# Performance work log

Measured on AMD Instinct MI355X. Metric: run time of the kernel, lower is better.

Reference implementation:

```python
import jax, jax.numpy as jnp
import numpy as np

GROUP_SIZE = 128
LORA_SCALING = 32.0 / 16.0  # lora_alpha / r


def _unpack_rows(q):
    # q: int32 [n, m] -> uint4 values [n*8, m], 8 nibbles per int32 along axis 0
    shifts = (jnp.arange(8, dtype=jnp.int32) * 4)
    vals = (q[:, None, :] >> shifts[None, :, None]) & 0xF
    return vals.reshape(q.shape[0] * 8, q.shape[1])


def _unpack_cols(q):
    # q: int32 [g, m] -> uint4 values [g, m*8], 8 nibbles per int32 along axis 1
    shifts = (jnp.arange(8, dtype=jnp.int32) * 4)
    vals = (q[:, :, None] >> shifts[None, None, :]) & 0xF
    return vals.reshape(q.shape[0], q.shape[1] * 8)


def setup_inputs() -> dict:
    key = jax.random.key(0)
    ks = jax.random.split(key, 6)
    in_f, out_f, tokens, r = 4096, 11008, 64, 16
    g = in_f // GROUP_SIZE  # 32 groups
    x = jax.random.normal(ks[0], (tokens, in_f), dtype=jnp.float32)
    qweight = jax.random.randint(ks[1], (in_f // 8, out_f), jnp.iinfo(jnp.int32).min, jnp.iinfo(jnp.int32).max, dtype=jnp.int32)
    qzeros = jax.random.randint(ks[2], (g, out_f // 8), jnp.iinfo(jnp.int32).min, jnp.iinfo(jnp.int32).max, dtype=jnp.int32)
    scales = jax.random.uniform(ks[3], (g, out_f), dtype=jnp.float32) * 0.01 + 0.001
    lora_A = jax.random.normal(ks[4], (r, in_f), dtype=jnp.float32) * 0.02
    lora_B = jax.random.normal(ks[5], (out_f, r), dtype=jnp.float32) * 0.02
    return {"x": x, "qweight": qweight, "qzeros": qzeros, "scales": scales,
            "lora_A": lora_A, "lora_B": lora_B}


def reference(x, qweight, qzeros, scales, lora_A, lora_B):
    in_f = qweight.shape[0] * 8
    # --- GPTQ int4 dequant ---
    wq = _unpack_rows(qweight).astype(jnp.float32)          # [in, out]
    zeros = (_unpack_cols(qzeros) + 1).astype(jnp.float32)  # [groups, out] (GPTQ +1 offset)
    g_idx = jnp.arange(in_f) // GROUP_SIZE                  # [in]
    W = scales[g_idx] * (wq - zeros[g_idx])                 # [in, out]
    # base quantized matmul
    result = x @ W                                          # [tokens, out]
    # --- LoRA adapter (single active adapter, dropout=0, tmp_weight=1) ---
    lora_out = (x @ lora_A.T) @ lora_B.T                    # [tokens, out]
    return result + lora_out * LORA_SCALING
```

## Files before the change

### kernel.cpp

```cpp
#include <hip/hip_runtime.h>
#include <stdint.h>

#define TOKENS 64
#define IN_F   4096
#define OUT_F  11008
#define RANK   16
#define GS     128
#define NG     32
#define ZCOLS  (OUT_F / 8)
#define LORA_SCALE 2.0f

using short8  = __attribute__((ext_vector_type(8))) short;
using float4v = __attribute__((ext_vector_type(4))) float;

static __device__ inline uint16_t f2bf(float f, float* back) {
    uint32_t u = __float_as_uint(f);
    uint32_t r = (u + 0x7FFFu + ((u >> 16) & 1u)) >> 16;
    *back = __uint_as_float(r << 16);
    return (uint16_t)r;
}

__global__ __launch_bounds__(256) void prep_kernel(
        const float* __restrict__ x,
        const float* __restrict__ loraA,
        uint4* __restrict__ xf4,
        float* __restrict__ xsumT,
        float* __restrict__ midT) {
    __shared__ float redg[256];
    __shared__ float redm[4][16];
    const int t    = blockIdx.x;
    const int tid  = threadIdx.x;
    const int lane = tid & 63;
    const int wv   = tid >> 6;

    float4 xv[4];
    const float4* xp = (const float4*)(x + (size_t)t * IN_F + tid * 16);
    #pragma unroll
    for (int i = 0; i < 4; ++i) xv[i] = xp[i];

    union { uint16_t u[16]; uint4 q[2]; } ob;
    float s = 0.f;
    #pragma unroll
    for (int i = 0; i < 4; ++i) {
        float b;
        ob.u[i * 4 + 0] = f2bf(xv[i].x, &b); s += b;
        ob.u[i * 4 + 1] = f2bf(xv[i].y, &b); s += b;
        ob.u[i * 4 + 2] = f2bf(xv[i].z, &b); s += b;
        ob.u[i * 4 + 3] = f2bf(xv[i].w, &b); s += b;
    }
    {
        const int mm = t >> 4, nn = t & 15;
        const int kchunk = tid >> 1;
        #pragma unroll
        for (int i = 0; i < 2; ++i) {
            const int qd = (tid * 2 + i) & 3;
            xf4[(size_t)((mm * 128 + kchunk) * 64 + qd * 16 + nn)] = ob.q[i];
        }
    }
    redg[tid] = s;

    float pj[16];
    #pragma unroll
    for (int j = 0; j < 16; ++j) {
        const float4* ap = (const float4*)(loraA + (size_t)j * IN_F + tid * 16);
        float ps = 0.f;
        #pragma unroll
        for (int i = 0; i < 4; ++i) {
            float4 a = ap[i];
            ps += a.x * xv[i].x + a.y * xv[i].y + a.z * xv[i].z + a.w * xv[i].w;
        }
        pj[j] = ps;
    }
    #pragma unroll
    for (int j = 0; j < 16; ++j) {
        #pragma unroll
        for (int off = 32; off; off >>= 1) pj[j] += __shfl_down(pj[j], off);
    }
    if (lane == 0) {
        #pragma unroll
        for (int j = 0; j < 16; ++j) redm[wv][j] = pj[j];
    }
    __syncthreads();
    if (tid < NG) {
        float g = 0.f;
        #pragma unroll
        for (int i = 0; i < 8; ++i) g += redg[tid * 8 + i];
        xsumT[tid * TOKENS + t] = g;
    }
    if (tid < 16)
        midT[tid * TOKENS + t] = redm[0][tid] + redm[1][tid] + redm[2][tid] + redm[3][tid];
}

__global__ __launch_bounds__(256) void lora_out_kernel(
        const float* __restrict__ midT,
        const float* __restrict__ loraB,
        float* __restrict__ out) {
    const int gid = blockIdx.x * 256 + threadIdx.x;
    const int t = gid / OUT_F;
    const int o = gid - t * OUT_F;
    const float4* b4 = (const float4*)(loraB + (size_t)o * RANK);
    float s = 0.f;
    #pragma unroll
    for (int i = 0; i < 4; ++i) {
        float4 b = b4[i];
        s += b.x * midT[(i * 4 + 0) * TOKENS + t];
        s += b.y * midT[(i * 4 + 1) * TOKENS + t];
        s += b.z * midT[(i * 4 + 2) * TOKENS + t];
        s += b.w * midT[(i * 4 + 3) * TOKENS + t];
    }
    out[gid] = s * LORA_SCALE;
}

#define LOADG(st, g) do {                                                       \
    _Pragma("unroll")                                                           \
    for (int mt = 0; mt < 2; ++mt)                                              \
        _Pragma("unroll")                                                       \
        for (int ks = 0; ks < 4; ++ks)                                          \
            A[st][mt * 4 + ks] =                                                \
                xf4[(size_t)(((mh * 2 + mt) * 128 + (g) * 4 + ks) * 64) + lane];\
    _Pragma("unroll")                                                           \
    for (int ks = 0; ks < 4; ++ks)                                              \
        _Pragma("unroll")                                                       \
        for (int nh = 0; nh < 2; ++nh)                                          \
            B[st][ks * 2 + nh] =                                                \
                qwc[(size_t)((g) * 16 + ks * 4 + quad) * OUT_F + nh * 16];      \
    _Pragma("unroll")                                                           \
    for (int mt = 0; mt < 2; ++mt)                                              \
        XS[st][mt] = *(const float4*)(xsumT + (g) * 64 +                        \
                                      (mh * 2 + mt) * 16 + quad * 4);           \
    _Pragma("unroll")                                                           \
    for (int nh = 0; nh < 2; ++nh) {                                            \
        S[st][nh] = scales[(size_t)(g) * OUT_F + col0 + nh * 16 + n];           \
        Z[st][nh] = qz[(size_t)(g) * ZCOLS + ((col0 + nh * 16 + n) >> 3)];      \
    }                                                                           \
} while (0)

#define COMPUTEG(st) do {                                                       \
    float4v accg[2][2];                                                         \
    _Pragma("unroll")                                                           \
    for (int mt = 0; mt < 2; ++mt)                                              \
        _Pragma("unroll")                                                       \
        for (int nh = 0; nh < 2; ++nh)                                          \
            accg[mt][nh] = (float4v){0.f, 0.f, 0.f, 0.f};                       \
    _Pragma("unroll")                                                           \
    for (int ks = 0; ks < 4; ++ks) {                                            \
        union { uint4 u; short8 s; } af0, af1;                                  \
        af0.u = A[st][ks];                                                      \
        af1.u = A[st][4 + ks];                                                  \
        _Pragma("unroll")                                                       \
        for (int nh = 0; nh < 2; ++nh) {                                        \
            uint32_t q  = B[st][ks * 2 + nh];                                   \
            uint32_t lo = q & 0x0F0F0F0Fu;                                      \
            uint32_t hi = (q >> 4) & 0x0F0F0F0Fu;                               \
            union { uint32_t u32[4]; short8 s8; } bf;                           \
            _Pragma("unroll")                                                   \
            for (int i = 0; i < 4; ++i)                                         \
                bf.u32[i] = __builtin_amdgcn_perm(hi, lo,                       \
                                0x0C040C00u + i * 0x00010001u) | 0x43004300u;   \
            accg[0][nh] = __builtin_amdgcn_mfma_f32_16x16x32_bf16(af0.s, bf.s8, \
                                                            accg[0][nh], 0, 0, 0);\
            accg[1][nh] = __builtin_amdgcn_mfma_f32_16x16x32_bf16(af1.s, bf.s8, \
                                                            accg[1][nh], 0, 0, 0);\
        }                                                                       \
    }                                                                           \
    _Pragma("unroll")                                                           \
    for (int nh = 0; nh < 2; ++nh) {                                            \
        const float zoff = (float)(((Z[st][nh] >>                               \
                        (((col0 + nh * 16 + n) & 7) * 4)) & 0xFu) + 129u);      \
        const float scl = S[st][nh];                                            \
        _Pragma("unroll")                                                       \
        for (int mt = 0; mt < 2; ++mt) {                                        \
            const float xr[4] = {XS[st][mt].x, XS[st][mt].y,                    \
                                 XS[st][mt].z, XS[st][mt].w};                   \
            _Pragma("unroll")                                                   \
            for (int r = 0; r < 4; ++r)                                         \
                acc[mt][nh][r] = fmaf(scl, fmaf(-zoff, xr[r],                   \
                                      accg[mt][nh][r]), acc[mt][nh][r]);        \
        }                                                                       \
    }                                                                           \
} while (0)

__global__ __launch_bounds__(256, 3) void main_kernel(
        const uint32_t* __restrict__ qw,
        const uint32_t* __restrict__ qz,
        const float* __restrict__ scales,
        const uint4* __restrict__ xf4,
        const float* __restrict__ xsumT,
        float* __restrict__ out) {
    const int tid  = threadIdx.x;
    const int wv   = tid >> 6;
    const int lane = tid & 63;
    const int n    = lane & 15;
    const int quad = lane >> 4;
    const int mh   = wv & 1;
    const int cs   = wv >> 1;
    const int colblk = blockIdx.x >> 2;
    const int kseg   = blockIdx.x & 3;
    const int col0   = colblk * 64 + cs * 32;
    const int g0     = kseg * 8;

    const uint32_t* qwc = qw + col0 + n;

    float4v acc[2][2];
    #pragma unroll
    for (int mt = 0; mt < 2; ++mt)
        #pragma unroll
        for (int nh = 0; nh < 2; ++nh)
            acc[mt][nh] = (float4v){0.f, 0.f, 0.f, 0.f};

    uint4    A[2][8];
    uint32_t B[2][8];
    float4   XS[2][2];
    float    S[2][2];
    uint32_t Z[2][2];

    LOADG(0, g0);
    LOADG(1, g0 + 1);
    #pragma unroll
    for (int gi = 0; gi < 8; ++gi) {
        const int st = gi & 1;
        COMPUTEG(st);
        int gl = gi + 2; if (gl > 7) gl = 7;
        LOADG(st, g0 + gl);
    }

    #pragma unroll
    for (int mt = 0; mt < 2; ++mt)
        #pragma unroll
        for (int nh = 0; nh < 2; ++nh)
            #pragma unroll
            for (int r = 0; r < 4; ++r) {
                const int t = (mh * 2 + mt) * 16 + quad * 4 + r;
                atomicAdd(out + (size_t)t * OUT_F + col0 + nh * 16 + n,
                          acc[mt][nh][r]);
            }
}

extern "C" void kernel_launch(void* const* d_in, const int* in_sizes, int n_in,
                              void* d_out, int out_size, void* d_ws, size_t ws_size,
                              hipStream_t stream) {
    const float*    x      = (const float*)d_in[0];
    const uint32_t* qw     = (const uint32_t*)d_in[1];
    const uint32_t* qz     = (const uint32_t*)d_in[2];
    const float*    scales = (const float*)d_in[3];
    const float*    loraA  = (const float*)d_in[4];
    const float*    loraB  = (const float*)d_in[5];
    float* out = (float*)d_out;

    uint4* xf4   = (uint4*)d_ws;
    float* xsumT = (float*)((char*)d_ws + (size_t)TOKENS * IN_F * 2);
    float* midT  = xsumT + NG * TOKENS;

    prep_kernel<<<TOKENS, 256, 0, stream>>>(x, loraA, xf4, xsumT, midT);
    lora_out_kernel<<<(TOKENS * OUT_F) / 256, 256, 0, stream>>>(midT, loraB, out);
    main_kernel<<<(OUT_F / 64) * 4, 256, 0, stream>>>(qw, qz, scales, xf4, xsumT, out);
}
```

Baseline: 107.2 us.

## Replace atomic split-K reduction with partial buffers and fused combine kernel

The main kernel now gives each block 32 output columns and has each of its four waves own 16 tokens, doubling the block count and raising the occupancy hint from 3 to 5. Instead of atomically adding split-K partials into the output, each K-segment writes its own partial buffer. A new combine kernel sums the four partials and adds the LoRA term, replacing the separate LoRA output kernel. This removes the atomic read-modify-write traffic, but costs extra workspace traffic (four partial writes and reads of the 64x11008 output) and halves B-operand reuse across the token dimension.

```diff
diff --git a/kernel.cpp b/kernel.cpp
--- a/kernel.cpp
+++ b/kernel.cpp
@@ -9,6 +9,8 @@
 #define NG     32
 #define ZCOLS  (OUT_F / 8)
 #define LORA_SCALE 2.0f
+#define KSEG 4
+#define GPK  (NG / KSEG)
 
 using short8  = __attribute__((ext_vector_type(8))) short;
 using float4v = __attribute__((ext_vector_type(4))) float;
@@ -91,33 +93,7 @@
         midT[tid * TOKENS + t] = redm[0][tid] + redm[1][tid] + redm[2][tid] + redm[3][tid];
 }
 
-__global__ __launch_bounds__(256) void lora_out_kernel(
-        const float* __restrict__ midT,
-        const float* __restrict__ loraB,
-        float* __restrict__ out) {
-    const int gid = blockIdx.x * 256 + threadIdx.x;
-    const int t = gid / OUT_F;
-    const int o = gid - t * OUT_F;
-    const float4* b4 = (const float4*)(loraB + (size_t)o * RANK);
-    float s = 0.f;
-    #pragma unroll
-    for (int i = 0; i < 4; ++i) {
-        float4 b = b4[i];
-        s += b.x * midT[(i * 4 + 0) * TOKENS + t];
-        s += b.y * midT[(i * 4 + 1) * TOKENS + t];
-        s += b.z * midT[(i * 4 + 2) * TOKENS + t];
-        s += b.w * midT[(i * 4 + 3) * TOKENS + t];
-    }
-    out[gid] = s * LORA_SCALE;
-}
-
 #define LOADG(st, g) do {                                                       \
-    _Pragma("unroll")                                                           \
-    for (int mt = 0; mt < 2; ++mt)                                              \
-        _Pragma("unroll")                                                       \
-        for (int ks = 0; ks < 4; ++ks)                                          \
-            A[st][mt * 4 + ks] =                                                \
-                xf4[(size_t)(((mh * 2 + mt) * 128 + (g) * 4 + ks) * 64) + lane];\
     _Pragma("unroll")                                                           \
     for (int ks = 0; ks < 4; ++ks)                                              \
         _Pragma("unroll")                                                       \
@@ -125,9 +101,9 @@
             B[st][ks * 2 + nh] =                                                \
                 qwc[(size_t)((g) * 16 + ks * 4 + quad) * OUT_F + nh * 16];      \
     _Pragma("unroll")                                                           \
-    for (int mt = 0; mt < 2; ++mt)                                              \
-        XS[st][mt] = *(const float4*)(xsumT + (g) * 64 +                        \
-                                      (mh * 2 + mt) * 16 + quad * 4);           \
+    for (int ks = 0; ks < 4; ++ks)                                              \
+        A[st][ks] = xf4[(size_t)((m * 128 + (g) * 4 + ks) * 64) + lane];        \
+    XS[st] = *(const float4*)(xsumT + (g) * 64 + m * 16 + quad * 4);            \
     _Pragma("unroll")                                                           \
     for (int nh = 0; nh < 2; ++nh) {                                            \
         S[st][nh] = scales[(size_t)(g) * OUT_F + col0 + nh * 16 + n];           \
@@ -136,17 +112,12 @@
 } while (0)
 
 #define COMPUTEG(st) do {                                                       \
-    float4v accg[2][2];                                                         \
-    _Pragma("unroll")                                                           \
-    for (int mt = 0; mt < 2; ++mt)                                              \
-        _Pragma("unroll")                                                       \
-        for (int nh = 0; nh < 2; ++nh)                                          \
-            accg[mt][nh] = (float4v){0.f, 0.f, 0.f, 0.f};                       \
+    float4v accg[2];                                                            \
+    accg[0] = (float4v){0.f, 0.f, 0.f, 0.f};                                    \
+    accg[1] = (float4v){0.f, 0.f, 0.f, 0.f};                                    \
     _Pragma("unroll")                                                           \
     for (int ks = 0; ks < 4; ++ks) {                                            \
-        union { uint4 u; short8 s; } af0, af1;                                  \
-        af0.u = A[st][ks];                                                      \
-        af1.u = A[st][4 + ks];                                                  \
+        union { uint4 u; short8 s; } afu; afu.u = A[st][ks];                    \
         _Pragma("unroll")                                                       \
         for (int nh = 0; nh < 2; ++nh) {                                        \
             uint32_t q  = B[st][ks * 2 + nh];                                   \
@@ -157,83 +128,96 @@
             for (int i = 0; i < 4; ++i)                                         \
                 bf.u32[i] = __builtin_amdgcn_perm(hi, lo,                       \
                                 0x0C040C00u + i * 0x00010001u) | 0x43004300u;   \
-            accg[0][nh] = __builtin_amdgcn_mfma_f32_16x16x32_bf16(af0.s, bf.s8, \
-                                                            accg[0][nh], 0, 0, 0);\
-            accg[1][nh] = __builtin_amdgcn_mfma_f32_16x16x32_bf16(af1.s, bf.s8, \
-                                                            accg[1][nh], 0, 0, 0);\
+            accg[nh] = __builtin_amdgcn_mfma_f32_16x16x32_bf16(afu.s, bf.s8,    \
+                                                            accg[nh], 0, 0, 0); \
         }                                                                       \
     }                                                                           \
+    const float xr[4] = {XS[st].x, XS[st].y, XS[st].z, XS[st].w};               \
     _Pragma("unroll")                                                           \
     for (int nh = 0; nh < 2; ++nh) {                                            \
         const float zoff = (float)(((Z[st][nh] >>                               \
                         (((col0 + nh * 16 + n) & 7) * 4)) & 0xFu) + 129u);      \
         const float scl = S[st][nh];                                            \
         _Pragma("unroll")                                                       \
-        for (int mt = 0; mt < 2; ++mt) {                                        \
-            const float xr[4] = {XS[st][mt].x, XS[st][mt].y,                    \
-                                 XS[st][mt].z, XS[st][mt].w};                   \
-            _Pragma("unroll")                                                   \
-            for (int r = 0; r < 4; ++r)                                         \
-                acc[mt][nh][r] = fmaf(scl, fmaf(-zoff, xr[r],                   \
-                                      accg[mt][nh][r]), acc[mt][nh][r]);        \
-        }                                                                       \
+        for (int r = 0; r < 4; ++r)                                             \
+            acc[nh][r] = fmaf(scl, fmaf(-zoff, xr[r], accg[nh][r]),             \
+                              acc[nh][r]);                                      \
     }                                                                           \
 } while (0)
 
-__global__ __launch_bounds__(256, 3) void main_kernel(
+__global__ __launch_bounds__(256, 5) void main_kernel(
         const uint32_t* __restrict__ qw,
         const uint32_t* __restrict__ qz,
         const float* __restrict__ scales,
         const uint4* __restrict__ xf4,
         const float* __restrict__ xsumT,
-        float* __restrict__ out) {
+        float* __restrict__ part) {
     const int tid  = threadIdx.x;
-    const int wv   = tid >> 6;
+    const int m    = tid >> 6;
     const int lane = tid & 63;
     const int n    = lane & 15;
     const int quad = lane >> 4;
-    const int mh   = wv & 1;
-    const int cs   = wv >> 1;
-    const int colblk = blockIdx.x >> 2;
-    const int kseg   = blockIdx.x & 3;
-    const int col0   = colblk * 64 + cs * 32;
-    const int g0     = kseg * 8;
+    const int cs   = blockIdx.x >> 2;
+    const int kseg = blockIdx.x & 3;
+    const int col0 = cs * 32;
+    const int g0   = kseg * GPK;
 
     const uint32_t* qwc = qw + col0 + n;
 
-    float4v acc[2][2];
-    #pragma unroll
-    for (int mt = 0; mt < 2; ++mt)
-        #pragma unroll
-        for (int nh = 0; nh < 2; ++nh)
-            acc[mt][nh] = (float4v){0.f, 0.f, 0.f, 0.f};
-
-    uint4    A[2][8];
+    float4v acc[2];
+    acc[0] = (float4v){0.f, 0.f, 0.f, 0.f};
+    acc[1] = (float4v){0.f, 0.f, 0.f, 0.f};
+
+    uint4    A[2][4];
     uint32_t B[2][8];
-    float4   XS[2][2];
+    float4   XS[2];
     float    S[2][2];
     uint32_t Z[2][2];
 
     LOADG(0, g0);
     LOADG(1, g0 + 1);
     #pragma unroll
-    for (int gi = 0; gi < 8; ++gi) {
+    for (int gi = 0; gi < GPK; ++gi) {
         const int st = gi & 1;
         COMPUTEG(st);
-        int gl = gi + 2; if (gl > 7) gl = 7;
-        LOADG(st, g0 + gl);
-    }
-
-    #pragma unroll
-    for (int mt = 0; mt < 2; ++mt)
-        #pragma unroll
-        for (int nh = 0; nh < 2; ++nh)
-            #pragma unroll
-            for (int r = 0; r < 4; ++r) {
-                const int t = (mh * 2 + mt) * 16 + quad * 4 + r;
-                atomicAdd(out + (size_t)t * OUT_F + col0 + nh * 16 + n,
-                          acc[mt][nh][r]);
-            }
+        if (gi + 2 < GPK) LOADG(st, g0 + gi + 2);
+    }
+
+    float* pp = part + (size_t)kseg * TOKENS * OUT_F;
+    #pragma unroll
+    for (int nh = 0; nh < 2; ++nh)
+        #pragma unroll
+        for (int r = 0; r < 4; ++r) {
+            const int t = m * 16 + quad * 4 + r;
+            pp[(size_t)t * OUT_F + col0 + nh * 16 + n] = acc[nh][r];
+        }
+}
+
+__global__ __launch_bounds__(256) void combine_kernel(
+        const float* __restrict__ part,
+        const float* __restrict__ midT,
+        const float* __restrict__ loraB,
+        float* __restrict__ out) {
+    const int gid = blockIdx.x * 256 + threadIdx.x;
+    const int t = gid / OUT_F;
+    const int o = gid - t * OUT_F;
+
+    float s = 0.f;
+    #pragma unroll
+    for (int ks = 0; ks < KSEG; ++ks)
+        s += part[(size_t)ks * TOKENS * OUT_F + gid];
+
+    const float4* b4 = (const float4*)(loraB + (size_t)o * RANK);
+    float ls = 0.f;
+    #pragma unroll
+    for (int i = 0; i < 4; ++i) {
+        float4 b = b4[i];
+        ls += b.x * midT[(i * 4 + 0) * TOKENS + t];
+        ls += b.y * midT[(i * 4 + 1) * TOKENS + t];
+        ls += b.z * midT[(i * 4 + 2) * TOKENS + t];
+        ls += b.w * midT[(i * 4 + 3) * TOKENS + t];
+    }
+    out[gid] = s + LORA_SCALE * ls;
 }
 
 extern "C" void kernel_launch(void* const* d_in, const int* in_sizes, int n_in,
@@ -250,8 +234,9 @@
     uint4* xf4   = (uint4*)d_ws;
     float* xsumT = (float*)((char*)d_ws + (size_t)TOKENS * IN_F * 2);
     float* midT  = xsumT + NG * TOKENS;
+    float* part  = midT + RANK * TOKENS;
 
     prep_kernel<<<TOKENS, 256, 0, stream>>>(x, loraA, xf4, xsumT, midT);
-    lora_out_kernel<<<(TOKENS * OUT_F) / 256, 256, 0, stream>>>(midT, loraB, out);
-    main_kernel<<<(OUT_F / 64) * 4, 256, 0, stream>>>(qw, qz, scales, xf4, xsumT, out);
-}
+    main_kernel<<<(OUT_F / 32) * KSEG, 256, 0, stream>>>(qw, qz, scales, xf4, xsumT, part);
+    combine_kernel<<<(TOKENS * OUT_F) / 256, 256, 0, stream>>>(part, midT, loraB, out);
+}
```

After: 120.3 us. +12.2%, slower.

## Fuse LoRA output and split-K reduction into main kernel via shared memory

Applied to the files above, without the earlier changes.

Drops the separate LoRA output kernel and the global atomicAdd split-K reduction. Each block now covers 32 columns with 8 waves: two token halves times four K segments. Partial sums are reduced through padded shared memory, the LoRA B projection is added, and the result is written once with float4 stores. The weight-load pipeline is deepened to triple-buffered B registers. The costs are a block-level sync, shared-memory use and higher register pressure at 512 threads, which may reduce occupancy.

```diff
diff --git a/kernel.cpp b/kernel.cpp
--- a/kernel.cpp
+++ b/kernel.cpp
@@ -9,6 +9,7 @@
 #define NG     32
 #define ZCOLS  (OUT_F / 8)
 #define LORA_SCALE 2.0f
+#define GPK 8
 
 using short8  = __attribute__((ext_vector_type(8))) short;
 using float4v = __attribute__((ext_vector_type(4))) float;
@@ -91,51 +92,37 @@
         midT[tid * TOKENS + t] = redm[0][tid] + redm[1][tid] + redm[2][tid] + redm[3][tid];
 }
 
-__global__ __launch_bounds__(256) void lora_out_kernel(
-        const float* __restrict__ midT,
-        const float* __restrict__ loraB,
-        float* __restrict__ out) {
-    const int gid = blockIdx.x * 256 + threadIdx.x;
-    const int t = gid / OUT_F;
-    const int o = gid - t * OUT_F;
-    const float4* b4 = (const float4*)(loraB + (size_t)o * RANK);
-    float s = 0.f;
-    #pragma unroll
-    for (int i = 0; i < 4; ++i) {
-        float4 b = b4[i];
-        s += b.x * midT[(i * 4 + 0) * TOKENS + t];
-        s += b.y * midT[(i * 4 + 1) * TOKENS + t];
-        s += b.z * midT[(i * 4 + 2) * TOKENS + t];
-        s += b.w * midT[(i * 4 + 3) * TOKENS + t];
-    }
-    out[gid] = s * LORA_SCALE;
-}
-
-#define LOADG(st, g) do {                                                       \
+#define PROW 34
+#define PIDX(mhv, ksv, tlv) (((mhv) * 4 + (ksv)) * (32 * PROW) + (tlv) * PROW)
+
+#define LOADB(sb, g) do {                                                       \
+    _Pragma("unroll")                                                           \
+    for (int ks = 0; ks < 4; ++ks)                                              \
+        _Pragma("unroll")                                                       \
+        for (int nh = 0; nh < 2; ++nh)                                          \
+            B[sb][ks * 2 + nh] =                                                \
+                qwc[(size_t)((g) * 16 + ks * 4 + quad) * OUT_F + nh * 16];      \
+} while (0)
+
+#define LOADA(sa, g) do {                                                       \
     _Pragma("unroll")                                                           \
     for (int mt = 0; mt < 2; ++mt)                                              \
         _Pragma("unroll")                                                       \
         for (int ks = 0; ks < 4; ++ks)                                          \
-            A[st][mt * 4 + ks] =                                                \
-                xf4[(size_t)(((mh * 2 + mt) * 128 + (g) * 4 + ks) * 64) + lane];\
-    _Pragma("unroll")                                                           \
-    for (int ks = 0; ks < 4; ++ks)                                              \
-        _Pragma("unroll")                                                       \
-        for (int nh = 0; nh < 2; ++nh)                                          \
-            B[st][ks * 2 + nh] =                                                \
-                qwc[(size_t)((g) * 16 + ks * 4 + quad) * OUT_F + nh * 16];      \
+            A[sa][mt * 4 + ks] =                                                \
+                xf4[(size_t)((((mh * 2 + mt) * 128 + (g) * 4 + ks) * 64)) + lane];\
     _Pragma("unroll")                                                           \
     for (int mt = 0; mt < 2; ++mt)                                              \
-        XS[st][mt] = *(const float4*)(xsumT + (g) * 64 +                        \
+        XS[sa][mt] = *(const float4*)(xsumT + (g) * 64 +                        \
                                       (mh * 2 + mt) * 16 + quad * 4);           \
     _Pragma("unroll")                                                           \
     for (int nh = 0; nh < 2; ++nh) {                                            \
-        S[st][nh] = scales[(size_t)(g) * OUT_F + col0 + nh * 16 + n];           \
-        Z[st][nh] = qz[(size_t)(g) * ZCOLS + ((col0 + nh * 16 + n) >> 3)];      \
+        S[sa][nh] = scales[(size_t)(g) * OUT_F + col0 + nh * 16 + n];           \
+        Z[sa][nh] = qz[(size_t)(g) * ZCOLS + ((col0 + nh * 16 + n) >> 3)];      \
     }                                                                           \
 } while (0)
 
-#define COMPUTEG(st) do {                                                       \
+#define COMPUTEG(sa, sb) do {                                                   \
     float4v accg[2][2];                                                         \
     _Pragma("unroll")                                                           \
     for (int mt = 0; mt < 2; ++mt)                                              \
@@ -145,11 +132,11 @@
     _Pragma("unroll")                                                           \
     for (int ks = 0; ks < 4; ++ks) {                                            \
         union { uint4 u; short8 s; } af0, af1;                                  \
-        af0.u = A[st][ks];                                                      \
-        af1.u = A[st][4 + ks];                                                  \
+        af0.u = A[sa][ks];                                                      \
+        af1.u = A[sa][4 + ks];                                                  \
         _Pragma("unroll")                                                       \
         for (int nh = 0; nh < 2; ++nh) {                                        \
-            uint32_t q  = B[st][ks * 2 + nh];                                   \
+            uint32_t q  = B[sb][ks * 2 + nh];                                   \
             uint32_t lo = q & 0x0F0F0F0Fu;                                      \
             uint32_t hi = (q >> 4) & 0x0F0F0F0Fu;                               \
             union { uint32_t u32[4]; short8 s8; } bf;                           \
@@ -165,13 +152,13 @@
     }                                                                           \
     _Pragma("unroll")                                                           \
     for (int nh = 0; nh < 2; ++nh) {                                            \
-        const float zoff = (float)(((Z[st][nh] >>                               \
+        const float zoff = (float)(((Z[sa][nh] >>                               \
                         (((col0 + nh * 16 + n) & 7) * 4)) & 0xFu) + 129u);      \
-        const float scl = S[st][nh];                                            \
+        const float scl = S[sa][nh];                                            \
         _Pragma("unroll")                                                       \
         for (int mt = 0; mt < 2; ++mt) {                                        \
-            const float xr[4] = {XS[st][mt].x, XS[st][mt].y,                    \
-                                 XS[st][mt].z, XS[st][mt].w};                   \
+            const float xr[4] = {XS[sa][mt].x, XS[sa][mt].y,                    \
+                                 XS[sa][mt].z, XS[sa][mt].w};                   \
             _Pragma("unroll")                                                   \
             for (int r = 0; r < 4; ++r)                                         \
                 acc[mt][nh][r] = fmaf(scl, fmaf(-zoff, xr[r],                   \
@@ -180,24 +167,26 @@
     }                                                                           \
 } while (0)
 
-__global__ __launch_bounds__(256, 3) void main_kernel(
+__global__ __launch_bounds__(512, 3) void main_kernel(
         const uint32_t* __restrict__ qw,
         const uint32_t* __restrict__ qz,
         const float* __restrict__ scales,
         const uint4* __restrict__ xf4,
         const float* __restrict__ xsumT,
+        const float* __restrict__ midT,
+        const float* __restrict__ loraB,
         float* __restrict__ out) {
+    __shared__ float part[2 * 4 * 32 * PROW];
+
     const int tid  = threadIdx.x;
     const int wv   = tid >> 6;
     const int lane = tid & 63;
     const int n    = lane & 15;
     const int quad = lane >> 4;
-    const int mh   = wv & 1;
-    const int cs   = wv >> 1;
-    const int colblk = blockIdx.x >> 2;
-    const int kseg   = blockIdx.x & 3;
-    const int col0   = colblk * 64 + cs * 32;
-    const int g0     = kseg * 8;
+    const int mh   = wv >> 2;
+    const int kseg = wv & 3;
+    const int col0 = blockIdx.x * 32;
+    const int g0   = kseg * GPK;
 
     const uint32_t* qwc = qw + col0 + n;
 
@@ -209,31 +198,72 @@
             acc[mt][nh] = (float4v){0.f, 0.f, 0.f, 0.f};
 
     uint4    A[2][8];
-    uint32_t B[2][8];
+    uint32_t B[3][8];
     float4   XS[2][2];
     float    S[2][2];
     uint32_t Z[2][2];
 
-    LOADG(0, g0);
-    LOADG(1, g0 + 1);
-    #pragma unroll
-    for (int gi = 0; gi < 8; ++gi) {
-        const int st = gi & 1;
-        COMPUTEG(st);
-        int gl = gi + 2; if (gl > 7) gl = 7;
-        LOADG(st, g0 + gl);
-    }
-
-    #pragma unroll
-    for (int mt = 0; mt < 2; ++mt)
-        #pragma unroll
-        for (int nh = 0; nh < 2; ++nh)
+    LOADB(0, g0); LOADB(1, g0 + 1); LOADB(2, g0 + 2);
+    LOADA(0, g0); LOADA(1, g0 + 1);
+    #pragma unroll
+    for (int gi = 0; gi < GPK; ++gi) {
+        const int sb = gi % 3, sa = gi & 1;
+        COMPUTEG(sa, sb);
+        if (gi + 3 < GPK) LOADB(sb, g0 + gi + 3);
+        if (gi + 2 < GPK) LOADA(sa, g0 + gi + 2);
+    }
+
+    {
+        float* pb = part + PIDX(mh, kseg, 0);
+        #pragma unroll
+        for (int mt = 0; mt < 2; ++mt)
             #pragma unroll
-            for (int r = 0; r < 4; ++r) {
-                const int t = (mh * 2 + mt) * 16 + quad * 4 + r;
-                atomicAdd(out + (size_t)t * OUT_F + col0 + nh * 16 + n,
-                          acc[mt][nh][r]);
+            for (int nh = 0; nh < 2; ++nh)
+                #pragma unroll
+                for (int r = 0; r < 4; ++r)
+                    pb[(mt * 16 + quad * 4 + r) * PROW + nh * 16 + n] =
+                        acc[mt][nh][r];
+    }
+    __syncthreads();
+
+    {
+        const int emh = tid >> 8;
+        const int rem = tid & 255;
+        const int tl  = rem >> 3;
+        const int c4  = (rem & 7) * 4;
+        const int t   = emh * 32 + tl;
+
+        float4 sum = *(const float4*)&part[PIDX(emh, 0, tl) + c4];
+        #pragma unroll
+        for (int ks = 1; ks < 4; ++ks) {
+            const float4 p = *(const float4*)&part[PIDX(emh, ks, tl) + c4];
+            sum.x += p.x; sum.y += p.y; sum.z += p.z; sum.w += p.w;
+        }
+
+        float m[16];
+        #pragma unroll
+        for (int j = 0; j < 16; ++j) m[j] = midT[j * TOKENS + t];
+        float ls[4];
+        #pragma unroll
+        for (int c = 0; c < 4; ++c) {
+            const float4* b4 = (const float4*)(loraB + (size_t)(col0 + c4 + c) * RANK);
+            float a = 0.f;
+            #pragma unroll
+            for (int i = 0; i < 4; ++i) {
+                float4 b = b4[i];
+                a += b.x * m[i * 4 + 0] + b.y * m[i * 4 + 1]
+                   + b.z * m[i * 4 + 2] + b.w * m[i * 4 + 3];
             }
+            ls[c] = a;
+        }
+
+        float4 o;
+        o.x = sum.x + LORA_SCALE * ls[0];
+        o.y = sum.y + LORA_SCALE * ls[1];
+        o.z = sum.z + LORA_SCALE * ls[2];
+        o.w = sum.w + LORA_SCALE * ls[3];
+        *(float4*)(out + (size_t)t * OUT_F + col0 + c4) = o;
+    }
 }
 
 extern "C" void kernel_launch(void* const* d_in, const int* in_sizes, int n_in,
@@ -252,6 +282,6 @@
     float* midT  = xsumT + NG * TOKENS;
 
     prep_kernel<<<TOKENS, 256, 0, stream>>>(x, loraA, xf4, xsumT, midT);
-    lora_out_kernel<<<(TOKENS * OUT_F) / 256, 256, 0, stream>>>(midT, loraB, out);
-    main_kernel<<<(OUT_F / 64) * 4, 256, 0, stream>>>(qw, qz, scales, xf4, xsumT, out);
-}
+    main_kernel<<<OUT_F / 32, 512, 0, stream>>>(qw, qz, scales, xf4, xsumT,
+                                                midT, loraB, out);
+}
```

Result: slower. 118.8 us (+10.9%).
